# Kernel tuning notes

Measured on AMD Instinct MI355X. Metric: run time of the kernel, lower is better.

The kernel has to match this reference:

```python
import jax, jax.numpy as jnp
from jax import lax
import numpy as np

NSTART, NOPEN, NHID, NCLOSE, NLAYERS, KSZ, N = 40, 128, 256, 3, 40, 9, 1024
H_STEP = 0.1
PAD = (KSZ - 1) // 2  # 4 -> same-length conv
EPS = 1e-5


def conv1(x, K):
    # x: (1, Cin, N), K: (Cout, Cin, k); cross-correlation like torch F.conv1d
    return lax.conv_general_dilated(x, K, (1,), [(PAD, PAD)],
                                    dimension_numbers=('NCH', 'OIH', 'NCH'))


def conv1T(x, K):
    # torch F.conv_transpose1d(x, K, padding=PAD) == conv1d with swapped-channel,
    # flipped kernel and padding k-1-PAD (= PAD here since k=9, PAD=4)
    Kt = jnp.flip(jnp.swapaxes(K, 0, 1), -1)
    return lax.conv_general_dilated(x, Kt, (1,), [(PAD, PAD)],
                                    dimension_numbers=('NCH', 'OIH', 'NCH'))


def instance_norm(x):
    # x: (1, C, N); normalize per channel over spatial dim, biased var, no affine
    m = jnp.mean(x, axis=-1, keepdims=True)
    v = jnp.var(x, axis=-1, keepdims=True)
    return (x - m) * lax.rsqrt(v + EPS)


def get_graph_lap(Z):
    # Z: (C, N). Normalized Gaussian-affinity graph Laplacian.
    sq = jnp.sum(Z * Z, axis=0)  # (N,)
    D2 = jnp.maximum(sq[:, None] + sq[None, :] - 2.0 * (Z.T @ Z), 0.0)
    sigma = jnp.mean(D2) + 1e-12
    Wg = jnp.exp(-D2 / sigma)
    deg = jnp.sum(Wg, axis=1)
    Dh = lax.rsqrt(deg)
    L = Dh[:, None] * (jnp.diag(deg) - Wg) * Dh[None, :]
    return L, deg


def double_sym_layer(Z, Wi, Bi, L):
    # Z: (nopen, N), Wi: (2, nhid, nopen, 9), Bi: (2, nopen, 1), L: (N, N)
    A0 = instance_norm(conv1((Z + Bi[0])[None], Wi[0]))
    A1 = instance_norm((conv1((Z + Bi[1])[None], Wi[1])[0] @ L)[None])
    A0 = jax.nn.relu(A0)
    A1 = jax.nn.relu(A1)
    A0 = conv1T(A0, Wi[0])[0]
    A1 = conv1T(A1, Wi[1])[0] @ L.T
    return A0 + A1  # (nopen, N)


def setup_inputs() -> dict:
    key = jax.random.key(0)
    k1, k2, k3, k4, k5 = jax.random.split(key, 5)
    Z = jax.random.normal(k1, (NSTART, N), dtype=jnp.float32)
    stdv_o = 0.001 * NOPEN / NSTART
    Kopen = jax.random.uniform(k2, (NOPEN, NSTART), minval=-stdv_o, maxval=stdv_o, dtype=jnp.float32)
    stdv_c = 0.001 * NCLOSE / NOPEN
    Kclose = jax.random.uniform(k3, (NCLOSE, NOPEN), minval=-stdv_c, maxval=stdv_c, dtype=jnp.float32)
    W = jax.random.uniform(k4, (NLAYERS, 2, NHID, NOPEN, KSZ), minval=-1e-4, maxval=1e-4, dtype=jnp.float32)
    Bias = jax.random.uniform(k5, (NLAYERS, 2, NOPEN, 1), dtype=jnp.float32) * 1e-4
    return {"Z": Z, "Kopen": Kopen, "Kclose": Kclose, "W": W, "Bias": Bias}


def reference(Z, Kopen, Kclose, W, Bias):
    h = H_STEP
    Zc = Kopen @ Z          # (nopen, N)
    Zold = Zc
    L, _ = get_graph_lap(Zc)
    for i in range(NLAYERS):
        if i % 10 == 0:
            L, _ = get_graph_lap(Zc)
        Ai = double_sym_layer(Zc, W[i], Bias[i], L)
        Zc, Zold = 2.0 * Zc - Zold - (h * h) * Ai, Zc  # leapfrog step
    return (Kclose @ Zc, Kclose @ Zold)
```

## Files before the change

kernel.cpp:

```cpp
#include <hip/hip_runtime.h>

#define NN 1024
#define NOPEN 128
#define NHID 256
#define NSTART 40
#define NCLOSE 3
#define NLAYERS 40
#define KSZ 9

static constexpr float H2 = 0.01f;
static constexpr float IN_EPS = 1e-5f;

using floatx4 = __attribute__((ext_vector_type(4))) float;
using bfrag = __attribute__((ext_vector_type(8))) short;

__device__ inline ushort f2bf(float f) {
    union { float f; unsigned u; } v; v.f = f;
    unsigned r = v.u + 0x7fffu + ((v.u >> 16) & 1u);
    return (ushort)(r >> 16);
}

__global__ void k_open(const float* __restrict__ Kopen, const float* __restrict__ Z,
                       float* __restrict__ Zc, float* __restrict__ Zold) {
    int n = blockIdx.x * 256 + threadIdx.x;
    int o = blockIdx.y;
    float acc = 0.f;
#pragma unroll
    for (int s = 0; s < NSTART; ++s)
        acc = fmaf(Kopen[o * NSTART + s], Z[s * NN + n], acc);
    Zc[o * NN + n] = acc;
    Zold[o * NN + n] = acc;
}

__global__ void k_sq(const float* __restrict__ Zc, float* __restrict__ sq, float* __restrict__ sig) {
    int i = blockIdx.x * 256 + threadIdx.x;
    float a = 0.f;
    for (int c = 0; c < NOPEN; ++c) { float v = Zc[c * NN + i]; a = fmaf(v, v, a); }
    sq[i] = a;
    if (i == 0) sig[0] = 0.f;
}

__global__ __launch_bounds__(256) void k_d2(const float* __restrict__ Zc, const float* __restrict__ sq,
                                            float* __restrict__ D2, float* __restrict__ sig) {
    __shared__ __align__(16) float Zi[32 * 36];
    __shared__ __align__(16) float Zj[32 * 68];
    __shared__ float red[4];
    const int tid = threadIdx.x;
    const int tx = tid & 15, ty = tid >> 4;
    const int j0 = blockIdx.x * 64, i0 = blockIdx.y * 32;
    float acc[2][4] = {};
    for (int c0 = 0; c0 < NOPEN; c0 += 32) {
        for (int idx = tid; idx < 32 * 32; idx += 256) {
            int c = idx >> 5, ii = idx & 31;
            Zi[c * 36 + ii] = Zc[(c0 + c) * NN + i0 + ii];
        }
        for (int idx = tid; idx < 32 * 64; idx += 256) {
            int c = idx >> 6, jj = idx & 63;
            Zj[c * 68 + jj] = Zc[(c0 + c) * NN + j0 + jj];
        }
        __syncthreads();
#pragma unroll 8
        for (int c = 0; c < 32; ++c) {
            float2 zi = *(const float2*)&Zi[c * 36 + ty * 2];
            float4 zj = *(const float4*)&Zj[c * 68 + tx * 4];
            acc[0][0] = fmaf(zi.x, zj.x, acc[0][0]);
            acc[0][1] = fmaf(zi.x, zj.y, acc[0][1]);
            acc[0][2] = fmaf(zi.x, zj.z, acc[0][2]);
            acc[0][3] = fmaf(zi.x, zj.w, acc[0][3]);
            acc[1][0] = fmaf(zi.y, zj.x, acc[1][0]);
            acc[1][1] = fmaf(zi.y, zj.y, acc[1][1]);
            acc[1][2] = fmaf(zi.y, zj.z, acc[1][2]);
            acc[1][3] = fmaf(zi.y, zj.w, acc[1][3]);
        }
        __syncthreads();
    }
    float part = 0.f;
#pragma unroll
    for (int m = 0; m < 2; ++m) {
        int i = i0 + ty * 2 + m;
        float sqi = sq[i];
        float4 d;
        d.x = fmaxf(sqi + sq[j0 + tx * 4 + 0] - 2.f * acc[m][0], 0.f);
        d.y = fmaxf(sqi + sq[j0 + tx * 4 + 1] - 2.f * acc[m][1], 0.f);
        d.z = fmaxf(sqi + sq[j0 + tx * 4 + 2] - 2.f * acc[m][2], 0.f);
        d.w = fmaxf(sqi + sq[j0 + tx * 4 + 3] - 2.f * acc[m][3], 0.f);
        *(float4*)&D2[(size_t)i * NN + j0 + tx * 4] = d;
        part += (d.x + d.y) + (d.z + d.w);
    }
#pragma unroll
    for (int off = 32; off > 0; off >>= 1) part += __shfl_down(part, off);
    if ((tid & 63) == 0) red[tid >> 6] = part;
    __syncthreads();
    if (tid == 0) atomicAdd(sig, red[0] + red[1] + red[2] + red[3]);
}

__global__ void k_deg(const float* __restrict__ D2, const float* __restrict__ sig,
                      float* __restrict__ Dh) {
    __shared__ float red[4];
    int i = blockIdx.x, tid = threadIdx.x;
    float inv = 1.f / (sig[0] * (1.f / 1048576.f) + 1e-12f);
    float4 v = *(const float4*)&D2[(size_t)i * NN + tid * 4];
    float s = __expf(-v.x * inv) + __expf(-v.y * inv) + __expf(-v.z * inv) + __expf(-v.w * inv);
#pragma unroll
    for (int off = 32; off > 0; off >>= 1) s += __shfl_down(s, off);
    if ((tid & 63) == 0) red[tid >> 6] = s;
    __syncthreads();
    if (tid == 0) Dh[i] = rsqrtf(red[0] + red[1] + red[2] + red[3]);
}

__global__ void k_L(const float* __restrict__ D2, const float* __restrict__ sig,
                    const float* __restrict__ Dh, ushort* __restrict__ Lb) {
    int i = blockIdx.x, tid = threadIdx.x;
    int j = tid * 4;
    float inv = 1.f / (sig[0] * (1.f / 1048576.f) + 1e-12f);
    float dhi = Dh[i];
    float4 v = *(const float4*)&D2[(size_t)i * NN + j];
    float4 dj = *(const float4*)&Dh[j];
    float4 o;
    o.x = -dhi * dj.x * __expf(-v.x * inv);
    o.y = -dhi * dj.y * __expf(-v.y * inv);
    o.z = -dhi * dj.z * __expf(-v.z * inv);
    o.w = -dhi * dj.w * __expf(-v.w * inv);
    if (i == j + 0) o.x += 1.f;
    if (i == j + 1) o.y += 1.f;
    if (i == j + 2) o.z += 1.f;
    if (i == j + 3) o.w += 1.f;
    ushort4 ob; ob.x = f2bf(o.x); ob.y = f2bf(o.y); ob.z = f2bf(o.z); ob.w = f2bf(o.w);
    *(ushort4*)&Lb[(size_t)i * NN + j] = ob;
}

__global__ __launch_bounds__(256) void k_prep(const float* __restrict__ Zc,
        const float* __restrict__ W, const float* __restrict__ B,
        ushort* __restrict__ Zct, ushort* __restrict__ Wt, ushort* __restrict__ WtT) {
    __shared__ ushort Ls[64 * 136];
    const int bb = blockIdx.x, tid = threadIdx.x;
    if (bb < 32) {
        const int z = bb >> 4, pt = bb & 15;
        const int p0 = pt * 64;
        const float* Bz = B + z * NOPEN;
#pragma unroll
        for (int r = 0; r < 8; ++r) {
            int idx = r * 256 + tid;
            int ci = idx >> 4, pq = idx & 15;
            float4 v = *(const float4*)&Zc[ci * NN + p0 + pq * 4];
            float bz = Bz[ci];
            Ls[(pq * 4 + 0) * 136 + ci] = f2bf(v.x + bz);
            Ls[(pq * 4 + 1) * 136 + ci] = f2bf(v.y + bz);
            Ls[(pq * 4 + 2) * 136 + ci] = f2bf(v.z + bz);
            Ls[(pq * 4 + 3) * 136 + ci] = f2bf(v.w + bz);
        }
        __syncthreads();
        ushort* Zz = Zct + z * (1032 * 128);
#pragma unroll
        for (int r = 0; r < 4; ++r) {
            int idx = r * 256 + tid;
            int row = idx >> 4, ch = (idx & 15) * 8;
            *(bfrag*)&Zz[(p0 + row + 4) * 128 + ch] = *(const bfrag*)&Ls[row * 136 + ch];
        }
        if (pt == 0)  for (int idx = tid; idx < 4 * 128; idx += 256) Zz[idx] = 0;
        if (pt == 15) for (int idx = tid; idx < 4 * 128; idx += 256) Zz[1028 * 128 + idx] = 0;
    } else if (bb < 104) {
        int q = bb - 32;
        const int coq = q & 3; q >>= 2;
        const int t = q % 9, z = q / 9;
        const float* Wz = W + z * (NHID * NOPEN * KSZ);
        ushort* Wo = Wt + (size_t)(z * 9 + t) * NHID * NOPEN;
#pragma unroll
        for (int r = 0; r < 32; ++r) {
            int idx = r * 256 + tid;
            int co = coq * 64 + (idx >> 7), ci = idx & 127;
            Wo[co * NOPEN + ci] = f2bf(Wz[co * (NOPEN * KSZ) + ci * KSZ + t]);
        }
    } else {
        int q = bb - 104;
        const int ciq = q & 3; q >>= 2;
        const int t = q % 9, z = q / 9;
        const float* Wz = W + z * (NHID * NOPEN * KSZ);
        ushort* Wo = WtT + (size_t)(z * 9 + t) * NOPEN * NHID;
#pragma unroll
        for (int r = 0; r < 32; ++r) {
            int idx = r * 256 + tid;
            int ci = ciq * 32 + (idx >> 8), co = idx & 255;
            Wo[ci * NHID + co] = f2bf(Wz[co * (NOPEN * KSZ) + ci * KSZ + t]);
        }
    }
}

__global__ __launch_bounds__(256) void k_conv(const ushort* __restrict__ Zct,
        const ushort* __restrict__ Wt, float* __restrict__ C0, ushort* __restrict__ C1b) {
    const int z = blockIdx.z;
    const int p0 = blockIdx.x * 64, co0 = blockIdx.y * 32;
    __shared__ ushort Xs[72 * 136];
    __shared__ ushort Wl[9 * 32 * 136];
    const int tid = threadIdx.x;
    const ushort* Zz = Zct + z * (1032 * 128);
    const ushort* Wz = Wt + (size_t)z * 9 * NHID * NOPEN;
    for (int idx = tid; idx < 1152; idx += 256) {
        int row = idx >> 4, ch = (idx & 15) * 8;
        *(bfrag*)&Xs[row * 136 + ch] = *(const bfrag*)&Zz[(p0 + row) * 128 + ch];
    }
    for (int idx = tid; idx < 4608; idx += 256) {
        int t = idx >> 9, rem = idx & 511;
        int c = rem >> 4, ch = (rem & 15) * 8;
        *(bfrag*)&Wl[(t * 32 + c) * 136 + ch] = *(const bfrag*)&Wz[(t * NHID + co0 + c) * 128 + ch];
    }
    __syncthreads();
    const int l = tid & 63, wv = tid >> 6;
    const int wm = wv >> 1, wn = wv & 1;
    const int lm = l & 15, lq = l >> 4;
    floatx4 acc[2] = {};
    for (int t = 0; t < 9; ++t) {
        const int wbase = (t * 32 + wm * 16 + lm) * 136 + lq * 8;
        const int xbase = (wn * 32 + lm + t) * 136 + lq * 8;
#pragma unroll
        for (int kc = 0; kc < 4; ++kc) {
            bfrag a = *(const bfrag*)&Wl[wbase + kc * 32];
            bfrag b0 = *(const bfrag*)&Xs[xbase + kc * 32];
            acc[0] = __builtin_amdgcn_mfma_f32_16x16x32_bf16(a, b0, acc[0], 0, 0, 0);
            bfrag b1 = *(const bfrag*)&Xs[xbase + 16 * 136 + kc * 32];
            acc[1] = __builtin_amdgcn_mfma_f32_16x16x32_bf16(a, b1, acc[1], 0, 0, 0);
        }
    }
    const int cog = co0 + wm * 16 + lq * 4;
    const int pg = p0 + wn * 32 + lm;
#pragma unroll
    for (int j = 0; j < 2; ++j)
#pragma unroll
        for (int r = 0; r < 4; ++r) {
            if (z == 0) C0[(cog + r) * NN + pg + j * 16] = acc[j][r];
            else        C1b[(cog + r) * NN + pg + j * 16] = f2bf(acc[j][r]);
        }
}

__global__ __launch_bounds__(256) void k_xl_mfma(const ushort* __restrict__ X,
                                                 const ushort* __restrict__ Lb,
                                                 float* __restrict__ P, int M) {
    __shared__ __align__(16) ushort As[64 * 136];
    __shared__ __align__(16) ushort Bs[128 * 136];
    const int tid = threadIdx.x;
    const int lane = tid & 63, wave = tid >> 6;
    const int wm = wave >> 1, wn = wave & 1;
    const int n0 = blockIdx.x * 128, m0 = blockIdx.y * 64, kc = blockIdx.z * 128;
    {
        int q = tid;
#pragma unroll
        for (int r = 0; r < 4; ++r, q += 256) {
            int row = q >> 4, ch = (q & 15) * 8;
            *(bfrag*)&As[row * 136 + ch] = *(const bfrag*)&X[(m0 + row) * NN + kc + ch];
        }
        q = tid;
#pragma unroll
        for (int r = 0; r < 8; ++r, q += 256) {
            int row = q >> 4, ch = (q & 15) * 8;
            *(bfrag*)&Bs[row * 136 + ch] = *(const bfrag*)&Lb[(n0 + row) * NN + kc + ch];
        }
    }
    __syncthreads();
    floatx4 acc[2][4] = {};
    const int lrow = (lane & 15) * 136;
    const int koff = (lane >> 4) * 8;
#pragma unroll
    for (int ks = 0; ks < 4; ++ks) {
        bfrag a[2], b[4];
#pragma unroll
        for (int i = 0; i < 2; ++i)
            a[i] = *(const bfrag*)&As[(wm * 32 + i * 16) * 136 + lrow + ks * 32 + koff];
#pragma unroll
        for (int j = 0; j < 4; ++j)
            b[j] = *(const bfrag*)&Bs[(wn * 64 + j * 16) * 136 + lrow + ks * 32 + koff];
#pragma unroll
        for (int i = 0; i < 2; ++i)
#pragma unroll
            for (int j = 0; j < 4; ++j)
                acc[i][j] = __builtin_amdgcn_mfma_f32_16x16x32_bf16(a[i], b[j], acc[i][j], 0, 0, 0);
    }
    const int mg0 = m0 + wm * 32 + (lane >> 4) * 4;
    const int ng0 = n0 + wn * 64 + (lane & 15);
    const size_t base = (size_t)blockIdx.z * M * NN;
#pragma unroll
    for (int i = 0; i < 2; ++i)
#pragma unroll
        for (int j = 0; j < 4; ++j)
#pragma unroll
            for (int r = 0; r < 4; ++r)
                P[base + (size_t)(mg0 + i * 16 + r) * NN + ng0 + j * 16] = acc[i][j][r];
}

__global__ void k_inorm(const float* __restrict__ C0, const float* __restrict__ P1,
                        float* __restrict__ A1sum, float* __restrict__ Mu, float* __restrict__ Rs) {
    const int c = blockIdx.x, arr = blockIdx.y, tid = threadIdx.x;
    __shared__ float rs[4], rq[4];
    float4 v;
    if (arr == 0) {
        v = *(const float4*)&C0[c * NN + tid * 4];
    } else {
        v.x = v.y = v.z = v.w = 0.f;
#pragma unroll
        for (int s = 0; s < 8; ++s) {
            float4 p = *(const float4*)&P1[(size_t)(s * NHID + c) * NN + tid * 4];
            v.x += p.x; v.y += p.y; v.z += p.z; v.w += p.w;
        }
        *(float4*)&A1sum[c * NN + tid * 4] = v;
    }
    float s = (v.x + v.y) + (v.z + v.w);
    float q = (v.x * v.x + v.y * v.y) + (v.z * v.z + v.w * v.w);
#pragma unroll
    for (int off = 32; off > 0; off >>= 1) { s += __shfl_down(s, off); q += __shfl_down(q, off); }
    if ((tid & 63) == 0) { rs[tid >> 6] = s; rq[tid >> 6] = q; }
    __syncthreads();
    if (tid == 0) {
        float S = rs[0] + rs[1] + rs[2] + rs[3];
        float Q = rq[0] + rq[1] + rq[2] + rq[3];
        float mean = S * (1.f / NN);
        float var = Q * (1.f / NN) - mean * mean;
        Mu[arr * NHID + c] = mean;
        Rs[arr * NHID + c] = rsqrtf(var + IN_EPS);
    }
}

__global__ __launch_bounds__(256) void k_normT(const float* __restrict__ C0,
        const float* __restrict__ A1sum, const float* __restrict__ Mu, const float* __restrict__ Rs,
        ushort* __restrict__ At0, ushort* __restrict__ At1) {
    const int arr = blockIdx.z;
    const int p0 = blockIdx.x * 64, co0 = blockIdx.y * 64;
    const float* in = arr ? A1sum : C0;
    ushort* out = arr ? At1 : At0;
    __shared__ ushort Ls[64 * 72];
    const int tid = threadIdx.x;
#pragma unroll
    for (int r = 0; r < 4; ++r) {
        int idx = r * 256 + tid;
        int col = idx >> 4, pq = idx & 15;
        int co = co0 + col;
        float4 v = *(const float4*)&in[co * NN + p0 + pq * 4];
        float m = Mu[arr * NHID + co], sc = Rs[arr * NHID + co];
        Ls[(pq * 4 + 0) * 72 + col] = f2bf(fmaxf((v.x - m) * sc, 0.f));
        Ls[(pq * 4 + 1) * 72 + col] = f2bf(fmaxf((v.y - m) * sc, 0.f));
        Ls[(pq * 4 + 2) * 72 + col] = f2bf(fmaxf((v.z - m) * sc, 0.f));
        Ls[(pq * 4 + 3) * 72 + col] = f2bf(fmaxf((v.w - m) * sc, 0.f));
    }
    __syncthreads();
#pragma unroll
    for (int r = 0; r < 2; ++r) {
        int idx = r * 256 + tid;
        int row = idx >> 3, ch = (idx & 7) * 8;
        *(bfrag*)&out[(p0 + row + 4) * 256 + co0 + ch] = *(const bfrag*)&Ls[row * 72 + ch];
    }
    if (blockIdx.y == 0) {
        if (blockIdx.x == 0)  for (int idx = tid; idx < 4 * 256; idx += 256) out[idx] = 0;
        if (blockIdx.x == 15) for (int idx = tid; idx < 4 * 256; idx += 256) out[1028 * 256 + idx] = 0;
    }
}

__global__ __launch_bounds__(256) void k_convT(const ushort* __restrict__ At0,
        const ushort* __restrict__ At1, const ushort* __restrict__ WtT,
        float* __restrict__ T0, ushort* __restrict__ T1b) {
    const int z = blockIdx.z;
    const int p0 = blockIdx.x * 64, ci0 = blockIdx.y * 16;
    __shared__ ushort Al[72 * 264];
    __shared__ ushort Wl[9 * 16 * 264];
    const ushort* A = z ? At1 : At0;
    const ushort* Wz = WtT + (size_t)z * 9 * NOPEN * NHID;
    const int tid = threadIdx.x;
    for (int idx = tid; idx < 2304; idx += 256) {
        int row = idx >> 5, ch = (idx & 31) * 8;
        *(bfrag*)&Al[row * 264 + ch] = *(const bfrag*)&A[(p0 + row) * 256 + ch];
    }
    for (int idx = tid; idx < 4608; idx += 256) {
        int t = idx >> 9, rem = idx & 511;
        int c = rem >> 5, ch = (rem & 31) * 8;
        *(bfrag*)&Wl[(t * 16 + c) * 264 + ch] = *(const bfrag*)&Wz[(t * NOPEN + ci0 + c) * 256 + ch];
    }
    __syncthreads();
    const int l = tid & 63, wv = tid >> 6;
    const int lm = l & 15, lq = l >> 4;
    floatx4 acc0 = {}, acc1 = {};
    for (int t = 0; t < 9; ++t) {
        const int abase = (wv * 16 + lm + 8 - t) * 264 + lq * 8;
        const int wbase = (t * 16 + lm) * 264 + lq * 8;
#pragma unroll
        for (int kc = 0; kc < 8; kc += 2) {
            bfrag a0 = *(const bfrag*)&Wl[wbase + kc * 32];
            bfrag b0 = *(const bfrag*)&Al[abase + kc * 32];
            acc0 = __builtin_amdgcn_mfma_f32_16x16x32_bf16(a0, b0, acc0, 0, 0, 0);
            bfrag a1 = *(const bfrag*)&Wl[wbase + kc * 32 + 32];
            bfrag b1 = *(const bfrag*)&Al[abase + kc * 32 + 32];
            acc1 = __builtin_amdgcn_mfma_f32_16x16x32_bf16(a1, b1, acc1, 0, 0, 0);
        }
    }
    floatx4 acc = acc0 + acc1;
    const int cig = ci0 + lq * 4;
    const int pg = p0 + wv * 16 + lm;
#pragma unroll
    for (int r = 0; r < 4; ++r) {
        if (z == 0) T0[(cig + r) * NN + pg] = acc[r];
        else        T1b[(cig + r) * NN + pg] = f2bf(acc[r]);
    }
}

__global__ void k_leap(const float* __restrict__ P2, const float* __restrict__ T0,
                       const float* __restrict__ Zc, float* __restrict__ Zold) {
    int off = (blockIdx.x * 256 + threadIdx.x) * 4;
    float4 a = *(const float4*)&T0[off];
#pragma unroll
    for (int s = 0; s < 8; ++s) {
        float4 p = *(const float4*)&P2[(size_t)(s << 17) + off];
        a.x += p.x; a.y += p.y; a.z += p.z; a.w += p.w;
    }
    float4 zc = *(const float4*)&Zc[off];
    float4 zo = *(const float4*)&Zold[off];
    float4 zn;
    zn.x = 2.f * zc.x - zo.x - H2 * a.x;
    zn.y = 2.f * zc.y - zo.y - H2 * a.y;
    zn.z = 2.f * zc.z - zo.z - H2 * a.z;
    zn.w = 2.f * zc.w - zo.w - H2 * a.w;
    *(float4*)&Zold[off] = zn;
}

__global__ void k_close(const float* __restrict__ Kclose, const float* __restrict__ Zc,
                        const float* __restrict__ Zold, float* __restrict__ out) {
    int n = blockIdx.x * 256 + threadIdx.x;
    int o = blockIdx.y;
    const float* Zb = blockIdx.z ? Zold : Zc;
    float a = 0.f;
#pragma unroll
    for (int c = 0; c < NOPEN; ++c) a = fmaf(Kclose[o * NOPEN + c], Zb[c * NN + n], a);
    out[blockIdx.z * (NCLOSE * NN) + o * NN + n] = a;
}

extern "C" void kernel_launch(void* const* d_in, const int* in_sizes, int n_in,
                              void* d_out, int out_size, void* d_ws, size_t ws_size,
                              hipStream_t stream) {
    const float* Z      = (const float*)d_in[0];
    const float* Kopen  = (const float*)d_in[1];
    const float* Kclose = (const float*)d_in[2];
    const float* W      = (const float*)d_in[3];
    const float* Bias   = (const float*)d_in[4];
    float* out = (float*)d_out;
    float* ws  = (float*)d_ws;

    float* Zb0   = ws + 0;
    float* Zb1   = ws + 131072;
    float* D2    = ws + 262144;
    float* C0    = ws + 1310720;
    float* A1sum = ws + 1572864;
    float* T0    = ws + 1835008;
    float* P1    = ws + 1966080;
    float* P2    = ws + 4063232;
    float* sq    = ws + 5111808;
    float* Dh    = ws + 5112832;
    float* sig   = ws + 5113856;
    float* Mu    = ws + 5114880;
    float* Rs    = ws + 5115904;
    ushort* Lb  = (ushort*)(ws + 5116928);
    ushort* C1b = (ushort*)(ws + 5641216);
    ushort* T1b = (ushort*)(ws + 5772288);
    ushort* Zct = (ushort*)(ws + 5837824);
    ushort* Wt  = (ushort*)(ws + 5969920);
    ushort* WtT = (ushort*)(ws + 6264832);
    ushort* At0 = (ushort*)(ws + 6559744);
    ushort* At1 = (ushort*)(ws + 6691840);

    k_open<<<dim3(4, NOPEN), 256, 0, stream>>>(Kopen, Z, Zb0, Zb1);

    float* Zc = Zb0;
    float* Zold = Zb1;
    for (int i = 0; i < NLAYERS; ++i) {
        if (i % 10 == 0) {
            k_sq<<<dim3(4), 256, 0, stream>>>(Zc, sq, sig);
            k_d2<<<dim3(16, 32), 256, 0, stream>>>(Zc, sq, D2, sig);
            k_deg<<<dim3(NN), 256, 0, stream>>>(D2, sig, Dh);
            k_L<<<dim3(NN), 256, 0, stream>>>(D2, sig, Dh, Lb);
        }
        const float* Wl = W + (size_t)i * 2 * NHID * NOPEN * KSZ;
        const float* Bl = Bias + (size_t)i * 2 * NOPEN;

        k_prep<<<dim3(176), 256, 0, stream>>>(Zc, Wl, Bl, Zct, Wt, WtT);
        k_conv<<<dim3(16, 8, 2), 256, 0, stream>>>(Zct, Wt, C0, C1b);
        k_xl_mfma<<<dim3(8, 4, 8), 256, 0, stream>>>(C1b, Lb, P1, NHID);
        k_inorm<<<dim3(NHID, 2), 256, 0, stream>>>(C0, P1, A1sum, Mu, Rs);
        k_normT<<<dim3(16, 4, 2), 256, 0, stream>>>(C0, A1sum, Mu, Rs, At0, At1);
        k_convT<<<dim3(16, 8, 2), 256, 0, stream>>>(At0, At1, WtT, T0, T1b);
        k_xl_mfma<<<dim3(8, 2, 8), 256, 0, stream>>>(T1b, Lb, P2, NOPEN);
        k_leap<<<dim3(128), 256, 0, stream>>>(P2, T0, Zc, Zold);
        float* tmp = Zc; Zc = Zold; Zold = tmp;
    }

    k_close<<<dim3(4, NCLOSE, 2), 256, 0, stream>>>(Kclose, Zc, Zold, out);
}
```

Measured before the change: 2.238 ms.

## Fuse per-layer prep into leapfrog kernel and cut split-K partial sums

Removes the separate prep, sq and inorm kernels. Bias-added bf16 conversion of Zc and next-layer weight repacking now run inside the leapfrog kernel, and squared norms are computed inside the D2 kernel. The X·L GEMM now splits K only 2 ways instead of 8, looping over K in smaller tiles, so the partial buffers and their reduction shrink. Instance-norm statistics move into the normalize/transpose kernel, which recomputes them per block. The risks are redundant stats reads across blocks, uncoalesced scattered bf16 stores in the leapfrog, and less GEMM parallelism.

Result: slower. 2.685 ms (+20.0%).

```diff
diff --git a/kernel.cpp b/kernel.cpp
--- a/kernel.cpp
+++ b/kernel.cpp
@@ -14,40 +14,83 @@
 using floatx4 = __attribute__((ext_vector_type(4))) float;
 using bfrag = __attribute__((ext_vector_type(8))) short;
 
-__device__ inline ushort f2bf(float f) {
+__device__ __forceinline__ ushort f2bf(float f) {
     union { float f; unsigned u; } v; v.f = f;
     unsigned r = v.u + 0x7fffu + ((v.u >> 16) & 1u);
     return (ushort)(r >> 16);
 }
 
-__global__ void k_open(const float* __restrict__ Kopen, const float* __restrict__ Z,
-                       float* __restrict__ Zc, float* __restrict__ Zold) {
-    int n = blockIdx.x * 256 + threadIdx.x;
-    int o = blockIdx.y;
-    float acc = 0.f;
-#pragma unroll
-    for (int s = 0; s < NSTART; ++s)
-        acc = fmaf(Kopen[o * NSTART + s], Z[s * NN + n], acc);
-    Zc[o * NN + n] = acc;
-    Zold[o * NN + n] = acc;
-}
-
-__global__ void k_sq(const float* __restrict__ Zc, float* __restrict__ sq, float* __restrict__ sig) {
-    int i = blockIdx.x * 256 + threadIdx.x;
-    float a = 0.f;
-    for (int c = 0; c < NOPEN; ++c) { float v = Zc[c * NN + i]; a = fmaf(v, v, a); }
-    sq[i] = a;
-    if (i == 0) sig[0] = 0.f;
-}
-
-__global__ __launch_bounds__(256) void k_d2(const float* __restrict__ Zc, const float* __restrict__ sq,
+__device__ __forceinline__ void prepw_piece(const float* __restrict__ W, ushort* __restrict__ Wt,
+                                            ushort* __restrict__ WtT, int lb, int lsrc, int tid) {
+    if (lb < 72) {
+        int q = lb; int coq = q & 3; q >>= 2; int t = q % 9, z = q / 9;
+        const float* Wz = W + (size_t)(lsrc * 2 + z) * (NHID * NOPEN * KSZ);
+        ushort* Wo = Wt + ((size_t)z * 9 + t) * (NHID * NOPEN);
+#pragma unroll
+        for (int r = 0; r < 32; ++r) {
+            int idx = r * 256 + tid;
+            int co = coq * 64 + (idx >> 7), ci = idx & 127;
+            Wo[co * NOPEN + ci] = f2bf(Wz[co * (NOPEN * KSZ) + ci * KSZ + t]);
+        }
+    } else {
+        int q = lb - 72; int ciq = q & 3; q >>= 2; int t = q % 9, z = q / 9;
+        const float* Wz = W + (size_t)(lsrc * 2 + z) * (NHID * NOPEN * KSZ);
+        ushort* Wo = WtT + ((size_t)z * 9 + t) * (NOPEN * NHID);
+#pragma unroll
+        for (int r = 0; r < 32; ++r) {
+            int idx = r * 256 + tid;
+            int ci = ciq * 32 + (idx >> 8), co = idx & 255;
+            Wo[ci * NHID + co] = f2bf(Wz[co * (NOPEN * KSZ) + ci * KSZ + t]);
+        }
+    }
+}
+
+__global__ __launch_bounds__(256) void k_open(const float* __restrict__ Kopen, const float* __restrict__ Z,
+                       float* __restrict__ Zc, float* __restrict__ Zold,
+                       const float* __restrict__ Bias0, ushort* __restrict__ Zct,
+                       ushort* __restrict__ At0, ushort* __restrict__ At1,
+                       const float* __restrict__ W, ushort* __restrict__ Wt,
+                       ushort* __restrict__ WtT, float* __restrict__ sig) {
+    const int v = blockIdx.x, tid = threadIdx.x;
+    if (v < 512) {
+        int o = v >> 2, n = (v & 3) * 256 + tid;
+        float acc = 0.f;
+#pragma unroll
+        for (int s = 0; s < NSTART; ++s)
+            acc = fmaf(Kopen[o * NSTART + s], Z[s * NN + n], acc);
+        Zc[o * NN + n] = acc;
+        Zold[o * NN + n] = acc;
+#pragma unroll
+        for (int z = 0; z < 2; ++z)
+            Zct[z * (1032 * 128) + (n + 4) * 128 + o] = f2bf(acc + Bias0[z * NOPEN + o]);
+    } else if (v < 656) {
+        prepw_piece(W, Wt, WtT, v - 512, 0, tid);
+    } else {
+        if (tid == 0) sig[0] = 0.f;
+        for (int idx = tid; idx < 1024; idx += 256) {
+            int z = idx >> 9, rr = idx & 511;
+            ushort* Zz = Zct + z * (1032 * 128);
+            Zz[rr] = 0; Zz[1028 * 128 + rr] = 0;
+        }
+        for (int idx = tid; idx < 2048; idx += 256) {
+            int a = idx >> 10, rr = idx & 1023;
+            ushort* A = a ? At1 : At0;
+            A[rr] = 0; A[1028 * 256 + rr] = 0;
+        }
+    }
+}
+
+__global__ __launch_bounds__(256) void k_d2(const float* __restrict__ Zc,
                                             float* __restrict__ D2, float* __restrict__ sig) {
     __shared__ __align__(16) float Zi[32 * 36];
     __shared__ __align__(16) float Zj[32 * 68];
+    __shared__ float sqi[32], sqj[64];
     __shared__ float red[4];
     const int tid = threadIdx.x;
     const int tx = tid & 15, ty = tid >> 4;
     const int j0 = blockIdx.x * 64, i0 = blockIdx.y * 32;
+    if (tid < 32) sqi[tid] = 0.f;
+    else if (tid < 96) sqj[tid - 32] = 0.f;
     float acc[2][4] = {};
     for (int c0 = 0; c0 < NOPEN; c0 += 32) {
         for (int idx = tid; idx < 32 * 32; idx += 256) {
@@ -59,6 +102,16 @@
             Zj[c * 68 + jj] = Zc[(c0 + c) * NN + j0 + jj];
         }
         __syncthreads();
+        if (tid < 32) {
+            float s = 0.f;
+            for (int c = 0; c < 32; ++c) { float x = Zi[c * 36 + tid]; s = fmaf(x, x, s); }
+            sqi[tid] += s;
+        } else if (tid < 96) {
+            int jj = tid - 32;
+            float s = 0.f;
+            for (int c = 0; c < 32; ++c) { float x = Zj[c * 68 + jj]; s = fmaf(x, x, s); }
+            sqj[jj] += s;
+        }
 #pragma unroll 8
         for (int c = 0; c < 32; ++c) {
             float2 zi = *(const float2*)&Zi[c * 36 + ty * 2];
@@ -78,12 +131,12 @@
 #pragma unroll
     for (int m = 0; m < 2; ++m) {
         int i = i0 + ty * 2 + m;
-        float sqi = sq[i];
+        float sqi_v = sqi[ty * 2 + m];
         float4 d;
-        d.x = fmaxf(sqi + sq[j0 + tx * 4 + 0] - 2.f * acc[m][0], 0.f);
-        d.y = fmaxf(sqi + sq[j0 + tx * 4 + 1] - 2.f * acc[m][1], 0.f);
-        d.z = fmaxf(sqi + sq[j0 + tx * 4 + 2] - 2.f * acc[m][2], 0.f);
-        d.w = fmaxf(sqi + sq[j0 + tx * 4 + 3] - 2.f * acc[m][3], 0.f);
+        d.x = fmaxf(sqi_v + sqj[tx * 4 + 0] - 2.f * acc[m][0], 0.f);
+        d.y = fmaxf(sqi_v + sqj[tx * 4 + 1] - 2.f * acc[m][1], 0.f);
+        d.z = fmaxf(sqi_v + sqj[tx * 4 + 2] - 2.f * acc[m][2], 0.f);
+        d.w = fmaxf(sqi_v + sqj[tx * 4 + 3] - 2.f * acc[m][3], 0.f);
         *(float4*)&D2[(size_t)i * NN + j0 + tx * 4] = d;
         part += (d.x + d.y) + (d.z + d.w);
     }
@@ -129,63 +182,6 @@
     *(ushort4*)&Lb[(size_t)i * NN + j] = ob;
 }
 
-__global__ __launch_bounds__(256) void k_prep(const float* __restrict__ Zc,
-        const float* __restrict__ W, const float* __restrict__ B,
-        ushort* __restrict__ Zct, ushort* __restrict__ Wt, ushort* __restrict__ WtT) {
-    __shared__ ushort Ls[64 * 136];
-    const int bb = blockIdx.x, tid = threadIdx.x;
-    if (bb < 32) {
-        const int z = bb >> 4, pt = bb & 15;
-        const int p0 = pt * 64;
-        const float* Bz = B + z * NOPEN;
-#pragma unroll
-        for (int r = 0; r < 8; ++r) {
-            int idx = r * 256 + tid;
-            int ci = idx >> 4, pq = idx & 15;
-            float4 v = *(const float4*)&Zc[ci * NN + p0 + pq * 4];
-            float bz = Bz[ci];
-            Ls[(pq * 4 + 0) * 136 + ci] = f2bf(v.x + bz);
-            Ls[(pq * 4 + 1) * 136 + ci] = f2bf(v.y + bz);
-            Ls[(pq * 4 + 2) * 136 + ci] = f2bf(v.z + bz);
-            Ls[(pq * 4 + 3) * 136 + ci] = f2bf(v.w + bz);
-        }
-        __syncthreads();
-        ushort* Zz = Zct + z * (1032 * 128);
-#pragma unroll
-        for (int r = 0; r < 4; ++r) {
-            int idx = r * 256 + tid;
-            int row = idx >> 4, ch = (idx & 15) * 8;
-            *(bfrag*)&Zz[(p0 + row + 4) * 128 + ch] = *(const bfrag*)&Ls[row * 136 + ch];
-        }
-        if (pt == 0)  for (int idx = tid; idx < 4 * 128; idx += 256) Zz[idx] = 0;
-        if (pt == 15) for (int idx = tid; idx < 4 * 128; idx += 256) Zz[1028 * 128 + idx] = 0;
-    } else if (bb < 104) {
-        int q = bb - 32;
-        const int coq = q & 3; q >>= 2;
-        const int t = q % 9, z = q / 9;
-        const float* Wz = W + z * (NHID * NOPEN * KSZ);
-        ushort* Wo = Wt + (size_t)(z * 9 + t) * NHID * NOPEN;
-#pragma unroll
-        for (int r = 0; r < 32; ++r) {
-            int idx = r * 256 + tid;
-            int co = coq * 64 + (idx >> 7), ci = idx & 127;
-            Wo[co * NOPEN + ci] = f2bf(Wz[co * (NOPEN * KSZ) + ci * KSZ + t]);
-        }
-    } else {
-        int q = bb - 104;
-        const int ciq = q & 3; q >>= 2;
-        const int t = q % 9, z = q / 9;
-        const float* Wz = W + z * (NHID * NOPEN * KSZ);
-        ushort* Wo = WtT + (size_t)(z * 9 + t) * NOPEN * NHID;
-#pragma unroll
-        for (int r = 0; r < 32; ++r) {
-            int idx = r * 256 + tid;
-            int ci = ciq * 32 + (idx >> 8), co = idx & 255;
-            Wo[ci * NHID + co] = f2bf(Wz[co * (NOPEN * KSZ) + ci * KSZ + t]);
-        }
-    }
-}
-
 __global__ __launch_bounds__(256) void k_conv(const ushort* __restrict__ Zct,
         const ushort* __restrict__ Wt, float* __restrict__ C0, ushort* __restrict__ C1b) {
     const int z = blockIdx.z;
@@ -232,129 +228,118 @@
         }
 }
 
-__global__ __launch_bounds__(256) void k_xl_mfma(const ushort* __restrict__ X,
-                                                 const ushort* __restrict__ Lb,
-                                                 float* __restrict__ P, int M) {
+__global__ __launch_bounds__(256) void k_xl(const ushort* __restrict__ X,
+        const ushort* __restrict__ Lb, float* __restrict__ P, int M) {
     __shared__ __align__(16) ushort As[64 * 136];
-    __shared__ __align__(16) ushort Bs[128 * 136];
+    __shared__ __align__(16) ushort Bs[64 * 136];
     const int tid = threadIdx.x;
     const int lane = tid & 63, wave = tid >> 6;
     const int wm = wave >> 1, wn = wave & 1;
-    const int n0 = blockIdx.x * 128, m0 = blockIdx.y * 64, kc = blockIdx.z * 128;
-    {
-        int q = tid;
-#pragma unroll
-        for (int r = 0; r < 4; ++r, q += 256) {
+    const int lm = lane & 15, lq = lane >> 4;
+    const int n0 = blockIdx.x * 64, m0 = blockIdx.y * 64, k0 = blockIdx.z * 512;
+    float* Out = P + (size_t)blockIdx.z * M * NN;
+    floatx4 acc[2][2] = {};
+    for (int kc = k0; kc < k0 + 512; kc += 128) {
+#pragma unroll
+        for (int r = 0; r < 4; ++r) {
+            int q = r * 256 + tid;
             int row = q >> 4, ch = (q & 15) * 8;
             *(bfrag*)&As[row * 136 + ch] = *(const bfrag*)&X[(m0 + row) * NN + kc + ch];
-        }
-        q = tid;
-#pragma unroll
-        for (int r = 0; r < 8; ++r, q += 256) {
-            int row = q >> 4, ch = (q & 15) * 8;
             *(bfrag*)&Bs[row * 136 + ch] = *(const bfrag*)&Lb[(n0 + row) * NN + kc + ch];
         }
-    }
-    __syncthreads();
-    floatx4 acc[2][4] = {};
-    const int lrow = (lane & 15) * 136;
-    const int koff = (lane >> 4) * 8;
-#pragma unroll
-    for (int ks = 0; ks < 4; ++ks) {
-        bfrag a[2], b[4];
-#pragma unroll
-        for (int i = 0; i < 2; ++i)
-            a[i] = *(const bfrag*)&As[(wm * 32 + i * 16) * 136 + lrow + ks * 32 + koff];
-#pragma unroll
-        for (int j = 0; j < 4; ++j)
-            b[j] = *(const bfrag*)&Bs[(wn * 64 + j * 16) * 136 + lrow + ks * 32 + koff];
-#pragma unroll
-        for (int i = 0; i < 2; ++i)
-#pragma unroll
-            for (int j = 0; j < 4; ++j)
-                acc[i][j] = __builtin_amdgcn_mfma_f32_16x16x32_bf16(a[i], b[j], acc[i][j], 0, 0, 0);
-    }
-    const int mg0 = m0 + wm * 32 + (lane >> 4) * 4;
-    const int ng0 = n0 + wn * 64 + (lane & 15);
-    const size_t base = (size_t)blockIdx.z * M * NN;
+        __syncthreads();
+#pragma unroll
+        for (int ks = 0; ks < 4; ++ks) {
+            bfrag a[2], b[2];
+#pragma unroll
+            for (int i = 0; i < 2; ++i)
+                a[i] = *(const bfrag*)&As[(wm * 32 + i * 16 + lm) * 136 + ks * 32 + lq * 8];
+#pragma unroll
+            for (int j = 0; j < 2; ++j)
+                b[j] = *(const bfrag*)&Bs[(wn * 32 + j * 16 + lm) * 136 + ks * 32 + lq * 8];
+#pragma unroll
+            for (int i = 0; i < 2; ++i)
+#pragma unroll
+                for (int j = 0; j < 2; ++j)
+                    acc[i][j] = __builtin_amdgcn_mfma_f32_16x16x32_bf16(a[i], b[j], acc[i][j], 0, 0, 0);
+        }
+        __syncthreads();
+    }
+    const int mg0 = m0 + wm * 32 + lq * 4;
+    const int ng0 = n0 + wn * 32 + lm;
 #pragma unroll
     for (int i = 0; i < 2; ++i)
 #pragma unroll
-        for (int j = 0; j < 4; ++j)
+        for (int j = 0; j < 2; ++j)
 #pragma unroll
             for (int r = 0; r < 4; ++r)
-                P[base + (size_t)(mg0 + i * 16 + r) * NN + ng0 + j * 16] = acc[i][j][r];
-}
-
-__global__ void k_inorm(const float* __restrict__ C0, const float* __restrict__ P1,
-                        float* __restrict__ A1sum, float* __restrict__ Mu, float* __restrict__ Rs) {
-    const int c = blockIdx.x, arr = blockIdx.y, tid = threadIdx.x;
-    __shared__ float rs[4], rq[4];
-    float4 v;
-    if (arr == 0) {
-        v = *(const float4*)&C0[c * NN + tid * 4];
-    } else {
-        v.x = v.y = v.z = v.w = 0.f;
-#pragma unroll
-        for (int s = 0; s < 8; ++s) {
-            float4 p = *(const float4*)&P1[(size_t)(s * NHID + c) * NN + tid * 4];
-            v.x += p.x; v.y += p.y; v.z += p.z; v.w += p.w;
-        }
-        *(float4*)&A1sum[c * NN + tid * 4] = v;
-    }
-    float s = (v.x + v.y) + (v.z + v.w);
-    float q = (v.x * v.x + v.y * v.y) + (v.z * v.z + v.w * v.w);
-#pragma unroll
-    for (int off = 32; off > 0; off >>= 1) { s += __shfl_down(s, off); q += __shfl_down(q, off); }
-    if ((tid & 63) == 0) { rs[tid >> 6] = s; rq[tid >> 6] = q; }
-    __syncthreads();
-    if (tid == 0) {
-        float S = rs[0] + rs[1] + rs[2] + rs[3];
-        float Q = rq[0] + rq[1] + rq[2] + rq[3];
+                Out[(size_t)(mg0 + i * 16 + r) * NN + ng0 + j * 16] = acc[i][j][r];
+}
+
+__global__ __launch_bounds__(256) void k_normT(const float* __restrict__ C0,
+        const float* __restrict__ A1, ushort* __restrict__ At0, ushort* __restrict__ At1) {
+    const int arr = blockIdx.z;
+    const int p0 = blockIdx.x * 64, co0 = blockIdx.y * 64;
+    const float* in = arr ? A1 : C0;
+    const float* in2 = arr ? A1 + (size_t)NHID * NN : nullptr;
+    ushort* out = arr ? At1 : At0;
+    __shared__ float ps[256], pqv[256], mu[64], rsx[64];
+    __shared__ ushort Ls[64 * 72];
+    const int tid = threadIdx.x;
+    {
+        const int ch = tid >> 2, q = tid & 3;
+        const float* row = in + (size_t)(co0 + ch) * NN;
+        const float* row2 = in2 ? in2 + (size_t)(co0 + ch) * NN : row;
+        float s = 0.f, qq = 0.f;
+        for (int j = 0; j < 64; ++j) {
+            int f = (j * 4 + q) * 4;
+            float4 v = *(const float4*)&row[f];
+            if (in2) {
+                float4 w = *(const float4*)&row2[f];
+                v.x += w.x; v.y += w.y; v.z += w.z; v.w += w.w;
+            }
+            s += (v.x + v.y) + (v.z + v.w);
+            qq += (v.x * v.x + v.y * v.y) + (v.z * v.z + v.w * v.w);
+        }
+        ps[ch * 4 + q] = s; pqv[ch * 4 + q] = qq;
+    }
+    __syncthreads();
+    if (tid < 64) {
+        float S = ps[tid * 4] + ps[tid * 4 + 1] + ps[tid * 4 + 2] + ps[tid * 4 + 3];
+        float Q = pqv[tid * 4] + pqv[tid * 4 + 1] + pqv[tid * 4 + 2] + pqv[tid * 4 + 3];
         float mean = S * (1.f / NN);
         float var = Q * (1.f / NN) - mean * mean;
-        Mu[arr * NHID + c] = mean;
-        Rs[arr * NHID + c] = rsqrtf(var + IN_EPS);
-    }
-}
-
-__global__ __launch_bounds__(256) void k_normT(const float* __restrict__ C0,
-        const float* __restrict__ A1sum, const float* __restrict__ Mu, const float* __restrict__ Rs,
-        ushort* __restrict__ At0, ushort* __restrict__ At1) {
-    const int arr = blockIdx.z;
-    const int p0 = blockIdx.x * 64, co0 = blockIdx.y * 64;
-    const float* in = arr ? A1sum : C0;
-    ushort* out = arr ? At1 : At0;
-    __shared__ ushort Ls[64 * 72];
-    const int tid = threadIdx.x;
+        mu[tid] = mean;
+        rsx[tid] = rsqrtf(var + IN_EPS);
+    }
+    __syncthreads();
 #pragma unroll
     for (int r = 0; r < 4; ++r) {
         int idx = r * 256 + tid;
-        int col = idx >> 4, pq = idx & 15;
-        int co = co0 + col;
-        float4 v = *(const float4*)&in[co * NN + p0 + pq * 4];
-        float m = Mu[arr * NHID + co], sc = Rs[arr * NHID + co];
-        Ls[(pq * 4 + 0) * 72 + col] = f2bf(fmaxf((v.x - m) * sc, 0.f));
-        Ls[(pq * 4 + 1) * 72 + col] = f2bf(fmaxf((v.y - m) * sc, 0.f));
-        Ls[(pq * 4 + 2) * 72 + col] = f2bf(fmaxf((v.z - m) * sc, 0.f));
-        Ls[(pq * 4 + 3) * 72 + col] = f2bf(fmaxf((v.w - m) * sc, 0.f));
+        int col = idx >> 4, pq2 = idx & 15;
+        float4 v = *(const float4*)(in + (size_t)(co0 + col) * NN + p0 + pq2 * 4);
+        if (in2) {
+            float4 w = *(const float4*)(in2 + (size_t)(co0 + col) * NN + p0 + pq2 * 4);
+            v.x += w.x; v.y += w.y; v.z += w.z; v.w += w.w;
+        }
+        float m = mu[col], sc = rsx[col];
+        Ls[(pq2 * 4 + 0) * 72 + col] = f2bf(fmaxf((v.x - m) * sc, 0.f));
+        Ls[(pq2 * 4 + 1) * 72 + col] = f2bf(fmaxf((v.y - m) * sc, 0.f));
+        Ls[(pq2 * 4 + 2) * 72 + col] = f2bf(fmaxf((v.z - m) * sc, 0.f));
+        Ls[(pq2 * 4 + 3) * 72 + col] = f2bf(fmaxf((v.w - m) * sc, 0.f));
     }
     __syncthreads();
 #pragma unroll
     for (int r = 0; r < 2; ++r) {
         int idx = r * 256 + tid;
-        int row = idx >> 3, ch = (idx & 7) * 8;
-        *(bfrag*)&out[(p0 + row + 4) * 256 + co0 + ch] = *(const bfrag*)&Ls[row * 72 + ch];
-    }
-    if (blockIdx.y == 0) {
-        if (blockIdx.x == 0)  for (int idx = tid; idx < 4 * 256; idx += 256) out[idx] = 0;
-        if (blockIdx.x == 15) for (int idx = tid; idx < 4 * 256; idx += 256) out[1028 * 256 + idx] = 0;
+        int row = idx >> 3, ch8 = (idx & 7) * 8;
+        *(bfrag*)&out[(size_t)(p0 + row + 4) * 256 + co0 + ch8] = *(const bfrag*)&Ls[row * 72 + ch8];
     }
 }
 
 __global__ __launch_bounds__(256) void k_convT(const ushort* __restrict__ At0,
         const ushort* __restrict__ At1, const ushort* __restrict__ WtT,
-        float* __restrict__ T0, ushort* __restrict__ T1b) {
+        float* __restrict__ Tacc, ushort* __restrict__ T1b) {
     const int z = blockIdx.z;
     const int p0 = blockIdx.x * 64, ci0 = blockIdx.y * 16;
     __shared__ ushort Al[72 * 264];
@@ -393,28 +378,46 @@
     const int pg = p0 + wv * 16 + lm;
 #pragma unroll
     for (int r = 0; r < 4; ++r) {
-        if (z == 0) T0[(cig + r) * NN + pg] = acc[r];
+        if (z == 0) Tacc[(cig + r) * NN + pg] = acc[r];
         else        T1b[(cig + r) * NN + pg] = f2bf(acc[r]);
     }
 }
 
-__global__ void k_leap(const float* __restrict__ P2, const float* __restrict__ T0,
-                       const float* __restrict__ Zc, float* __restrict__ Zold) {
-    int off = (blockIdx.x * 256 + threadIdx.x) * 4;
-    float4 a = *(const float4*)&T0[off];
-#pragma unroll
-    for (int s = 0; s < 8; ++s) {
-        float4 p = *(const float4*)&P2[(size_t)(s << 17) + off];
-        a.x += p.x; a.y += p.y; a.z += p.z; a.w += p.w;
-    }
-    float4 zc = *(const float4*)&Zc[off];
-    float4 zo = *(const float4*)&Zold[off];
-    float4 zn;
-    zn.x = 2.f * zc.x - zo.x - H2 * a.x;
-    zn.y = 2.f * zc.y - zo.y - H2 * a.y;
-    zn.z = 2.f * zc.z - zo.z - H2 * a.z;
-    zn.w = 2.f * zc.w - zo.w - H2 * a.w;
-    *(float4*)&Zold[off] = zn;
+__global__ __launch_bounds__(256) void k_leap(const float* __restrict__ A2,
+        const float* __restrict__ Tacc, const float* __restrict__ Zc, float* __restrict__ Zo,
+        const float* __restrict__ BiasN, ushort* __restrict__ Zct,
+        const float* __restrict__ W, ushort* __restrict__ Wt, ushort* __restrict__ WtT,
+        float* __restrict__ sig, int lnext, int doprep) {
+    const int v = blockIdx.x, tid = threadIdx.x;
+    if (v < 128) {
+        int off = (v * 256 + tid) * 4;
+        float4 a = *(const float4*)&Tacc[off];
+        float4 q0 = *(const float4*)&A2[off];
+        float4 q1 = *(const float4*)&A2[NOPEN * NN + off];
+        a.x += q0.x + q1.x; a.y += q0.y + q1.y; a.z += q0.z + q1.z; a.w += q0.w + q1.w;
+        float4 zc = *(const float4*)&Zc[off];
+        float4 zo = *(const float4*)&Zo[off];
+        float4 zn;
+        zn.x = 2.f * zc.x - zo.x - H2 * a.x;
+        zn.y = 2.f * zc.y - zo.y - H2 * a.y;
+        zn.z = 2.f * zc.z - zo.z - H2 * a.z;
+        zn.w = 2.f * zc.w - zo.w - H2 * a.w;
+        *(float4*)&Zo[off] = zn;
+        int ci = off >> 10, n = off & 1023;
+#pragma unroll
+        for (int z = 0; z < 2; ++z) {
+            float bz = BiasN[z * NOPEN + ci];
+            ushort* Zz = Zct + z * (1032 * 128);
+            Zz[(n + 4) * 128 + ci] = f2bf(zn.x + bz);
+            Zz[(n + 5) * 128 + ci] = f2bf(zn.y + bz);
+            Zz[(n + 6) * 128 + ci] = f2bf(zn.z + bz);
+            Zz[(n + 7) * 128 + ci] = f2bf(zn.w + bz);
+        }
+    } else if (v < 272) {
+        if (doprep) prepw_piece(W, Wt, WtT, v - 128, lnext, tid);
+    } else {
+        if (tid == 0) sig[0] = 0.f;
+    }
 }
 
 __global__ void k_close(const float* __restrict__ Kclose, const float* __restrict__ Zc,
@@ -439,50 +442,44 @@
     float* out = (float*)d_out;
     float* ws  = (float*)d_ws;
 
-    float* Zb0   = ws + 0;
-    float* Zb1   = ws + 131072;
-    float* D2    = ws + 262144;
-    float* C0    = ws + 1310720;
-    float* A1sum = ws + 1572864;
-    float* T0    = ws + 1835008;
-    float* P1    = ws + 1966080;
-    float* P2    = ws + 4063232;
-    float* sq    = ws + 5111808;
-    float* Dh    = ws + 5112832;
-    float* sig   = ws + 5113856;
-    float* Mu    = ws + 5114880;
-    float* Rs    = ws + 5115904;
-    ushort* Lb  = (ushort*)(ws + 5116928);
-    ushort* C1b = (ushort*)(ws + 5641216);
-    ushort* T1b = (ushort*)(ws + 5772288);
-    ushort* Zct = (ushort*)(ws + 5837824);
-    ushort* Wt  = (ushort*)(ws + 5969920);
-    ushort* WtT = (ushort*)(ws + 6264832);
-    ushort* At0 = (ushort*)(ws + 6559744);
-    ushort* At1 = (ushort*)(ws + 6691840);
-
-    k_open<<<dim3(4, NOPEN), 256, 0, stream>>>(Kopen, Z, Zb0, Zb1);
+    float* Zb0  = ws + 0;
+    float* Zb1  = ws + 131072;
+    float* D2   = ws + 262144;
+    float* C0   = ws + 1310720;
+    float* A1   = ws + 1572864;
+    float* A2   = ws + 2097152;
+    float* Tacc = ws + 2359296;
+    float* Dh   = ws + 2490368;
+    float* sig  = ws + 2491392;
+    ushort* Lb  = (ushort*)(ws + 2492416);
+    ushort* C1b = (ushort*)(ws + 3016704);
+    ushort* T1b = (ushort*)(ws + 3147776);
+    ushort* Zct = (ushort*)(ws + 3213312);
+    ushort* At0 = (ushort*)(ws + 3345408);
+    ushort* At1 = (ushort*)(ws + 3477504);
+    ushort* Wt  = (ushort*)(ws + 3609600);
+    ushort* WtT = (ushort*)(ws + 3904512);
+
+    k_open<<<dim3(657), 256, 0, stream>>>(Kopen, Z, Zb0, Zb1, Bias, Zct, At0, At1,
+                                          W, Wt, WtT, sig);
 
     float* Zc = Zb0;
     float* Zold = Zb1;
     for (int i = 0; i < NLAYERS; ++i) {
         if (i % 10 == 0) {
-            k_sq<<<dim3(4), 256, 0, stream>>>(Zc, sq, sig);
-            k_d2<<<dim3(16, 32), 256, 0, stream>>>(Zc, sq, D2, sig);
+            k_d2<<<dim3(16, 32), 256, 0, stream>>>(Zc, D2, sig);
             k_deg<<<dim3(NN), 256, 0, stream>>>(D2, sig, Dh);
             k_L<<<dim3(NN), 256, 0, stream>>>(D2, sig, Dh, Lb);
         }
-        const float* Wl = W + (size_t)i * 2 * NHID * NOPEN * KSZ;
-        const float* Bl = Bias + (size_t)i * 2 * NOPEN;
-
-        k_prep<<<dim3(176), 256, 0, stream>>>(Zc, Wl, Bl, Zct, Wt, WtT);
         k_conv<<<dim3(16, 8, 2), 256, 0, stream>>>(Zct, Wt, C0, C1b);
-        k_xl_mfma<<<dim3(8, 4, 8), 256, 0, stream>>>(C1b, Lb, P1, NHID);
-        k_inorm<<<dim3(NHID, 2), 256, 0, stream>>>(C0, P1, A1sum, Mu, Rs);
-        k_normT<<<dim3(16, 4, 2), 256, 0, stream>>>(C0, A1sum, Mu, Rs, At0, At1);
-        k_convT<<<dim3(16, 8, 2), 256, 0, stream>>>(At0, At1, WtT, T0, T1b);
-        k_xl_mfma<<<dim3(8, 2, 8), 256, 0, stream>>>(T1b, Lb, P2, NOPEN);
-        k_leap<<<dim3(128), 256, 0, stream>>>(P2, T0, Zc, Zold);
+        k_xl<<<dim3(16, 4, 2), 256, 0, stream>>>(C1b, Lb, A1, NHID);
+        k_normT<<<dim3(16, 4, 2), 256, 0, stream>>>(C0, A1, At0, At1);
+        k_convT<<<dim3(16, 8, 2), 256, 0, stream>>>(At0, At1, WtT, Tacc, T1b);
+        k_xl<<<dim3(16, 2, 2), 256, 0, stream>>>(T1b, Lb, A2, NOPEN);
+        int lnext = (i + 1 < NLAYERS) ? i + 1 : NLAYERS - 1;
+        k_leap<<<dim3(273), 256, 0, stream>>>(A2, Tacc, Zc, Zold,
+                                              Bias + (size_t)lnext * 2 * NOPEN, Zct,
+                                              W, Wt, WtT, sig, lnext, (i + 1 < NLAYERS) ? 1 : 0);
         float* tmp = Zc; Zc = Zold; Zold = tmp;
     }
 
```
